# Optimization experiments

Hardware: AMD Instinct MI355X
Metric: run time of the kernel (lower is better)

Reference implementation:

```python
import jax, jax.numpy as jnp
import numpy as np

N, E, EE = 2048, 32768, 262144
CS, CZ, CG, NRBF = 384, 128, 16, 64
D_MIN, D_MAX = 0.0, 20.0
LN_EPS = 1e-5
EPS = 1e-8


def _p(key, shape, scale):
    return (jax.random.normal(key, shape, dtype=jnp.float32) * scale)


def setup_inputs() -> dict:
    key = jax.random.key(0)
    ks = jax.random.split(key, 40)
    inp = {
        "node_features": jax.random.normal(ks[0], (N, CS), dtype=jnp.float32),
        "node_trans": jax.random.normal(ks[1], (N, 3), dtype=jnp.float32) * 5.0,
        "dst_edge_features": jax.random.normal(ks[2], (E, CZ), dtype=jnp.float32),
        "dst_edge_index": jax.random.randint(ks[3], (2, E), 0, N),
        "src_edge_features": jax.random.normal(ks[4], (E, CZ), dtype=jnp.float32),
        "src_edge_index": jax.random.randint(ks[5], (2, E), 0, N),
        "edge_edge_index": jax.random.randint(ks[6], (2, EE), 0, E),
        # params (torch Linear math: y = x @ W + b, W stored [in,out])
        "w_nl": _p(ks[7], (CS, CG), 0.05), "b_nl": jnp.zeros((CG,), jnp.float32),
        "w_nr": _p(ks[8], (CS, CG), 0.05), "b_nr": jnp.zeros((CG,), jnp.float32),
        "g_dst": jnp.ones((CZ,), jnp.float32), "bt_dst": jnp.zeros((CZ,), jnp.float32),
        "g_src": jnp.ones((CZ,), jnp.float32), "bt_src": jnp.zeros((CZ,), jnp.float32),
        "w_ep": _p(ks[9], (CZ, CZ), 0.08), "b_ep": jnp.zeros((CZ,), jnp.float32),
        "w_eg": _p(ks[10], (CZ, CZ), 0.08), "b_eg": jnp.zeros((CZ,), jnp.float32),
        "w_dg": _p(ks[11], (CG * CG, CZ), 0.06), "b_dg": jnp.zeros((CZ,), jnp.float32),
        "w_dp": _p(ks[12], (NRBF, CZ), 0.1), "b_dp": jnp.zeros((CZ,), jnp.float32),
        "g_out": jnp.ones((CZ,), jnp.float32), "bt_out": jnp.zeros((CZ,), jnp.float32),
        "w_lo": _p(ks[13], (CZ, CZ), 0.08), "b_lo": jnp.zeros((CZ,), jnp.float32),
        "w_og": _p(ks[14], (CZ, CZ), 0.08), "b_og": jnp.zeros((CZ,), jnp.float32),
    }
    return inp


def _ln(x, g, b):
    m = jnp.mean(x, axis=-1, keepdims=True)
    v = jnp.mean(jnp.square(x - m), axis=-1, keepdims=True)
    return (x - m) * jax.lax.rsqrt(v + LN_EPS) * g + b


def _rbf(d):
    mu = jnp.linspace(D_MIN, D_MAX, NRBF)  # [NRBF]
    sigma = (D_MAX - D_MIN) / NRBF
    return jnp.exp(-jnp.square((d[:, None] - mu) / sigma))  # [EE, NRBF]


def reference(node_features, node_trans, dst_edge_features, dst_edge_index,
              src_edge_features, src_edge_index, edge_edge_index,
              w_nl, b_nl, w_nr, b_nr, g_dst, bt_dst, g_src, bt_src,
              w_ep, b_ep, w_eg, b_eg, w_dg, b_dg, w_dp, b_dp,
              g_out, bt_out, w_lo, b_lo, w_og, b_og):
    ee0 = edge_edge_index[0]  # index into dst edges
    ee1 = edge_edge_index[1]  # index into src edges
    n1 = src_edge_index[0][ee1]  # left node per edge-edge pair
    n2 = dst_edge_index[0][ee0]  # right node per edge-edge pair

    dst_ef = _ln(dst_edge_features, g_dst, bt_dst)
    src_ef = _ln(src_edge_features, g_src, bt_src)

    node_left = node_features @ w_nl + b_nl   # [N, CG]
    node_right = node_features @ w_nr + b_nr  # [N, CG]

    # per-pair outer product gate: [EE, CG*CG]
    edge3 = jnp.einsum('ei,ej->eij', node_left[n1], node_right[n2]).reshape(-1, CG * CG)
    edge3_gate = edge3 @ w_dg + b_dg  # [EE, CZ]

    diff = node_trans[n1] - node_trans[n2] + EPS
    dist = jnp.linalg.norm(diff, axis=-1)  # [EE]
    dist_feat = _rbf(dist) @ w_dp + b_dp   # [EE, CZ]
    edge3_features = jax.nn.sigmoid(edge3_gate) * dist_feat

    edge2 = jax.nn.sigmoid(src_ef @ w_eg + b_eg) * (src_ef @ w_ep + b_ep)  # [E, CZ]
    edge_update = edge2[ee0] * edge3_features  # [EE, CZ]
    edge_update = jax.ops.segment_sum(edge_update, ee0, num_segments=E)  # [E, CZ]

    edge_update = _ln(edge_update, g_out, bt_out)
    edge_update = edge_update @ w_lo + b_lo
    edge_update = edge_update * jax.nn.sigmoid(dst_ef @ w_og + b_og)
    return edge_update
```

## Files before the change

kernel.cpp:

```cpp
#include <hip/hip_runtime.h>
#include <hip/hip_bf16.h>
#include <math.h>

#define NN    2048
#define NE    32768
#define NP    262144
#define CS_   384
#define CZ_   128
#define CG_   16
#define NRBF_ 64

typedef __attribute__((ext_vector_type(8))) short bf16x8;
typedef __attribute__((ext_vector_type(4))) float f32x4;

__device__ __forceinline__ unsigned short f2bf(float f) {
  __hip_bfloat16 h = __float2bfloat16(f);
  union { __hip_bfloat16 h; unsigned short u; } cv; cv.h = h; return cv.u;
}
__device__ __forceinline__ float bfbits(unsigned short h) {
  return __uint_as_float((unsigned)h << 16);
}
__device__ __forceinline__ float sigf(float x) {
  return __builtin_amdgcn_rcpf(1.f + __expf(-x));
}

__global__ void k_nodeproj(const float* __restrict__ nf,
                           const float* __restrict__ wnl, const float* __restrict__ bnl,
                           const float* __restrict__ wnr, const float* __restrict__ bnr,
                           unsigned short* __restrict__ nl, unsigned short* __restrict__ nr) {
  const int n = blockIdx.x;
  const int t = threadIdx.x;
  if (t >= 32) return;
  const float* __restrict__ w = (t < 16) ? wnl : wnr;
  const int col = t & 15;
  const float* __restrict__ row = nf + (size_t)n * CS_;
  float acc = 0.f;
  #pragma unroll 8
  for (int k = 0; k < CS_; ++k) acc = fmaf(row[k], w[k * CG_ + col], acc);
  acc += (t < 16) ? bnl[col] : bnr[col];
  ((t < 16) ? nl : nr)[n * CG_ + col] = f2bf(acc);
}

__global__ void k_prep(const float* __restrict__ wdg, const float* __restrict__ wdp,
                       const float* __restrict__ weg, const float* __restrict__ wep,
                       const float* __restrict__ wlo, const float* __restrict__ wog,
                       unsigned short* __restrict__ frag) {
  const int idx = blockIdx.x * 256 + threadIdx.x;
  if (idx >= 180224) return;
  if (idx < 32768) {
    const int e = idx & 7, l = (idx >> 3) & 63, ks = (idx >> 9) & 7, n = idx >> 12;
    frag[idx] = f2bf(wdg[(size_t)(ks * 32 + (l >> 4) * 8 + e) * CZ_ + n * 16 + (l & 15)]);
  } else if (idx < 40960) {
    const int j = idx - 32768;
    const int e = j & 7, l = (j >> 3) & 63, ks2 = (j >> 9) & 1, n = j >> 10;
    frag[idx] = f2bf(wdp[(size_t)(ks2 * 32 + (l >> 4) * 8 + e) * CZ_ + n * 16 + (l & 15)]);
  } else if (idx < 172032) {
    const bool lo = idx >= 106496;
    const int j2 = (idx - 40960) & 65535;
    const int m = j2 >> 14;
    const float* __restrict__ mp = (m == 0) ? weg : (m == 1) ? wep : (m == 2) ? wlo : wog;
    const int j = j2 & 16383;
    const int e = j & 7, l = (j >> 3) & 63, ks = (j >> 9) & 3, n = j >> 11;
    const float v = mp[(size_t)(ks * 32 + (l >> 4) * 8 + e) * CZ_ + n * 16 + (l & 15)];
    const unsigned short h = f2bf(v);
    frag[idx] = lo ? f2bf(v - bfbits(h)) : h;
  } else {
    const int j = idx - 172032;
    const int e = j & 7, l = (j >> 3) & 63, ks2 = (j >> 9) & 1, n = j >> 10;
    const float v = wdp[(size_t)(ks2 * 32 + (l >> 4) * 8 + e) * CZ_ + n * 16 + (l & 15)];
    const unsigned short h = f2bf(v);
    frag[idx] = f2bf(v - bfbits(h));
  }
}

__global__ void k_hist(const int* __restrict__ ee, int* __restrict__ hist) {
  const int p = blockIdx.x * 256 + threadIdx.x;
  atomicAdd(&hist[ee[p]], 1);
}

__global__ __launch_bounds__(1024) void k_scan(int* __restrict__ hist,
                                               int* __restrict__ start) {
  __shared__ int tot[1024];
  const int t = threadIdx.x;
  const int base = t * 32;
  int s = 0;
  for (int k = 0; k < 32; ++k) s += hist[base + k];
  tot[t] = s;
  __syncthreads();
  for (int off = 1; off < 1024; off <<= 1) {
    int v = tot[t];
    int u = (t >= off) ? tot[t - off] : 0;
    __syncthreads();
    tot[t] = v + u;
    __syncthreads();
  }
  int run = (t == 0) ? 0 : tot[t - 1];
  for (int k = 0; k < 32; ++k) {
    const int h = hist[base + k];
    start[base + k] = run;
    run += h;
    hist[base + k] = 0;
  }
  if (t == 1023) start[32768] = run;
}

__global__ void k_scatter(const int* __restrict__ ee, const int* __restrict__ start,
                          int* __restrict__ cursor, int* __restrict__ perm) {
  const int p = blockIdx.x * 256 + threadIdx.x;
  const int e = ee[p];
  const int idx = atomicAdd(&cursor[e], 1);
  perm[start[e] + idx] = p;
}

__device__ __forceinline__ void ln_to_frag2(
    const float* __restrict__ src, const float* __restrict__ gam,
    const float* __restrict__ bet, int row0, int tid,
    unsigned short (* __restrict__ afh)[64][8],
    unsigned short (* __restrict__ afl)[64][8]) {
  const int r = tid >> 2, qt = tid & 3;
  const float* __restrict__ xp = src + (size_t)(row0 + r) * CZ_ + qt * 32;
  float v[32];
  #pragma unroll
  for (int j = 0; j < 8; ++j) {
    const float4 t4 = ((const float4*)xp)[j];
    v[4*j+0] = t4.x; v[4*j+1] = t4.y; v[4*j+2] = t4.z; v[4*j+3] = t4.w;
  }
  float sum = 0.f, sq = 0.f;
  #pragma unroll
  for (int q = 0; q < 32; ++q) { sum += v[q]; sq = fmaf(v[q], v[q], sq); }
  sum += __shfl_xor(sum, 1); sq += __shfl_xor(sq, 1);
  sum += __shfl_xor(sum, 2); sq += __shfl_xor(sq, 2);
  const float mean = sum * (1.f / CZ_);
  const float rstd = rsqrtf(sq * (1.f / CZ_) - mean * mean + 1e-5f);
  const int fb = (r >> 4) * 4 + qt;
  const int r15 = r & 15;
  #pragma unroll
  for (int g = 0; g < 4; ++g) {
    unsigned pkh[4], pkl[4];
    #pragma unroll
    for (int h2 = 0; h2 < 4; ++h2) {
      const int c0 = qt * 32 + g * 8 + 2 * h2;
      const float f0 = (v[g*8+2*h2]   - mean) * rstd * gam[c0]   + bet[c0];
      const float f1 = (v[g*8+2*h2+1] - mean) * rstd * gam[c0+1] + bet[c0+1];
      const unsigned short h0 = f2bf(f0), h1 = f2bf(f1);
      const unsigned short l0 = f2bf(f0 - bfbits(h0)), l1 = f2bf(f1 - bfbits(h1));
      pkh[h2] = (unsigned)h0 | ((unsigned)h1 << 16);
      pkl[h2] = (unsigned)l0 | ((unsigned)l1 << 16);
    }
    *(uint4*)&afh[fb][g * 16 + r15][0] = make_uint4(pkh[0], pkh[1], pkh[2], pkh[3]);
    *(uint4*)&afl[fb][g * 16 + r15][0] = make_uint4(pkl[0], pkl[1], pkl[2], pkl[3]);
  }
}

__global__ __launch_bounds__(256) void k_edge2_mfma(
    const float* __restrict__ sef,
    const float* __restrict__ gs, const float* __restrict__ bs,
    const unsigned short* __restrict__ wf,
    const float* __restrict__ beg, const float* __restrict__ bep,
    float* __restrict__ e2) {
  __shared__ unsigned short afh[16][64][8];
  __shared__ unsigned short afl[16][64][8];
  const int tid = threadIdx.x;
  const int row0 = blockIdx.x * 64;
  ln_to_frag2(sef, gs, bs, row0, tid, afh, afl);
  __syncthreads();

  const int lane = tid & 63;
  const int w = tid >> 6;
  f32x4 c1[8], c2[8];
  #pragma unroll
  for (int n = 0; n < 8; ++n) { c1[n] = (f32x4)0.f; c2[n] = (f32x4)0.f; }
  #pragma unroll
  for (int ks = 0; ks < 4; ++ks) {
    const bf16x8 ah = *(const bf16x8*)&afh[w * 4 + ks][lane][0];
    const bf16x8 al = *(const bf16x8*)&afl[w * 4 + ks][lane][0];
    #pragma unroll
    for (int n = 0; n < 8; ++n) {
      const size_t bo = ((size_t)((n * 4 + ks) * 64 + lane)) * 8;
      const bf16x8 b1h = *(const bf16x8*)(wf + bo);
      const bf16x8 b1l = *(const bf16x8*)(wf + 65536 + bo);
      const bf16x8 b2h = *(const bf16x8*)(wf + 16384 + bo);
      const bf16x8 b2l = *(const bf16x8*)(wf + 81920 + bo);
      c1[n] = __builtin_amdgcn_mfma_f32_16x16x32_bf16(ah, b1h, c1[n], 0, 0, 0);
      c1[n] = __builtin_amdgcn_mfma_f32_16x16x32_bf16(al, b1h, c1[n], 0, 0, 0);
      c1[n] = __builtin_amdgcn_mfma_f32_16x16x32_bf16(ah, b1l, c1[n], 0, 0, 0);
      c2[n] = __builtin_amdgcn_mfma_f32_16x16x32_bf16(ah, b2h, c2[n], 0, 0, 0);
      c2[n] = __builtin_amdgcn_mfma_f32_16x16x32_bf16(al, b2h, c2[n], 0, 0, 0);
      c2[n] = __builtin_amdgcn_mfma_f32_16x16x32_bf16(ah, b2l, c2[n], 0, 0, 0);
    }
  }
  const int c15 = lane & 15, rq = lane >> 4;
  #pragma unroll
  for (int n = 0; n < 8; ++n) {
    const int ch = n * 16 + c15;
    const float bg = beg[ch], bp = bep[ch];
    #pragma unroll
    for (int r = 0; r < 4; ++r) {
      const int row = row0 + w * 16 + rq * 4 + r;
      e2[(size_t)row * CZ_ + ch] = sigf(c1[n][r] + bg) * (c2[n][r] + bp);
    }
  }
}

template <int CC>
__global__ __launch_bounds__(256, 2) void k_pairfeat(
    const int* __restrict__ ee,
    const int* __restrict__ sei, const int* __restrict__ dei,
    const unsigned short* __restrict__ nlb, const unsigned short* __restrict__ nrb,
    const float* __restrict__ trans, const unsigned short* __restrict__ frag,
    const float* __restrict__ bdg, const float* __restrict__ bdp,
    float* __restrict__ feat) {
  __shared__ unsigned short sfrag[20480];
  const int tid = threadIdx.x;

  {
    const unsigned short* __restrict__ gsrc = frag + CC * 16384;
    #pragma unroll
    for (int i = 0; i < 8; ++i)
      ((float4*)sfrag)[i * 256 + tid] = ((const float4*)gsrc)[i * 256 + tid];
    const unsigned short* __restrict__ rsrc = frag + 32768 + CC * 4096;
    #pragma unroll
    for (int i = 0; i < 2; ++i)
      ((float4*)(sfrag + 16384))[i * 256 + tid] = ((const float4*)rsrc)[i * 256 + tid];
  }
  const unsigned short* __restrict__ wf2l = frag + 172032 + CC * 4096;

  const int lane = tid & 63;
  const int w = tid >> 6;
  const int g = lane >> 4;
  const int c15 = lane & 15;
  const int rowbase = blockIdx.x * 128 + w * 32;

  unsigned int nlu[2][8], nru[2][8];
  float dist[2];
  #pragma unroll
  for (int m = 0; m < 2; ++m) {
    const int p = rowbase + m * 16 + c15;
    const int e0 = ee[p];
    const int e1 = ee[NP + p];
    const int n1 = sei[e1];
    const int n2 = dei[e0];
    const uint4 a = ((const uint4*)(nlb + (size_t)n1 * CG_))[0];
    const uint4 b = ((const uint4*)(nlb + (size_t)n1 * CG_))[1];
    nlu[m][0]=a.x; nlu[m][1]=a.y; nlu[m][2]=a.z; nlu[m][3]=a.w;
    nlu[m][4]=b.x; nlu[m][5]=b.y; nlu[m][6]=b.z; nlu[m][7]=b.w;
    const uint4 c = ((const uint4*)(nrb + (size_t)n2 * CG_))[0];
    const uint4 d = ((const uint4*)(nrb + (size_t)n2 * CG_))[1];
    nru[m][0]=c.x; nru[m][1]=c.y; nru[m][2]=c.z; nru[m][3]=c.w;
    nru[m][4]=d.x; nru[m][5]=d.y; nru[m][6]=d.z; nru[m][7]=d.w;
    const float dx = trans[n1*3+0] - trans[n2*3+0] + 1e-8f;
    const float dy = trans[n1*3+1] - trans[n2*3+1] + 1e-8f;
    const float dz = trans[n1*3+2] - trans[n2*3+2] + 1e-8f;
    dist[m] = sqrtf(fmaf(dx, dx, fmaf(dy, dy, dz * dz)));
  }
  __syncthreads();

  f32x4 acc[2][4], acc2[2][4];
  #pragma unroll
  for (int m = 0; m < 2; ++m)
    #pragma unroll
    for (int n = 0; n < 4; ++n) { acc[m][n] = (f32x4)0.f; acc2[m][n] = (f32x4)0.f; }

  const bool hiI = (lane & 32) != 0;
  const bool hiJ = (lane & 16) != 0;

  #pragma unroll
  for (int ks = 0; ks < 8; ++ks) {
    bf16x8 af[2];
    #pragma unroll
    for (int m = 0; m < 2; ++m) {
      const unsigned wv = nlu[m][ks];
      const float nli = __uint_as_float(hiI ? (wv & 0xFFFF0000u) : (wv << 16));
      #pragma unroll
      for (int ep = 0; ep < 4; ++ep) {
        const unsigned wr = hiJ ? nru[m][4 + ep] : nru[m][ep];
        const float j0 = __uint_as_float(wr << 16);
        const float j1 = __uint_as_float(wr & 0xFFFF0000u);
        af[m][2*ep]   = (short)f2bf(nli * j0);
        af[m][2*ep+1] = (short)f2bf(nli * j1);
      }
    }
    #pragma unroll
    for (int n = 0; n < 4; ++n) {
      const bf16x8 bf = *(const bf16x8*)(sfrag + ((size_t)((n * 8 + ks) * 64 + lane)) * 8);
      acc[0][n] = __builtin_amdgcn_mfma_f32_16x16x32_bf16(af[0], bf, acc[0][n], 0, 0, 0);
      acc[1][n] = __builtin_amdgcn_mfma_f32_16x16x32_bf16(af[1], bf, acc[1][n], 0, 0, 0);
    }
  }

  const float MU_STEP = 20.f / 63.f;
  const float INV_SIG = 64.f / 20.f;
  #pragma unroll
  for (int ks2 = 0; ks2 < 2; ++ks2) {
    bf16x8 a2h[2], a2l[2];
    const int k2b = ks2 * 32 + g * 8;
    #pragma unroll
    for (int m = 0; m < 2; ++m) {
      #pragma unroll
      for (int e = 0; e < 8; ++e) {
        const float mu = (float)(k2b + e) * MU_STEP;
        const float u = (dist[m] - mu) * INV_SIG;
        const float ev = __expf(-u * u);
        const unsigned short h = f2bf(ev);
        a2h[m][e] = (short)h;
        a2l[m][e] = (short)f2bf(ev - bfbits(h));
      }
    }
    #pragma unroll
    for (int n = 0; n < 4; ++n) {
      const size_t bo = ((size_t)((n * 2 + ks2) * 64 + lane)) * 8;
      const bf16x8 b2h = *(const bf16x8*)(sfrag + 16384 + bo);
      const bf16x8 b2l = *(const bf16x8*)(wf2l + bo);
      acc2[0][n] = __builtin_amdgcn_mfma_f32_16x16x32_bf16(a2h[0], b2h, acc2[0][n], 0, 0, 0);
      acc2[0][n] = __builtin_amdgcn_mfma_f32_16x16x32_bf16(a2l[0], b2h, acc2[0][n], 0, 0, 0);
      acc2[0][n] = __builtin_amdgcn_mfma_f32_16x16x32_bf16(a2h[0], b2l, acc2[0][n], 0, 0, 0);
      acc2[1][n] = __builtin_amdgcn_mfma_f32_16x16x32_bf16(a2h[1], b2h, acc2[1][n], 0, 0, 0);
      acc2[1][n] = __builtin_amdgcn_mfma_f32_16x16x32_bf16(a2l[1], b2h, acc2[1][n], 0, 0, 0);
      acc2[1][n] = __builtin_amdgcn_mfma_f32_16x16x32_bf16(a2h[1], b2l, acc2[1][n], 0, 0, 0);
    }
  }

  float bdgv[4], bdpv[4];
  #pragma unroll
  for (int n = 0; n < 4; ++n) {
    bdgv[n] = bdg[(CC * 4 + n) * 16 + c15];
    bdpv[n] = bdp[(CC * 4 + n) * 16 + c15];
  }

  #pragma unroll
  for (int m = 0; m < 2; ++m) {
    #pragma unroll
    for (int n = 0; n < 4; ++n) {
      #pragma unroll
      for (int r = 0; r < 4; ++r) {
        const float gv = sigf(acc[m][n][r] + bdgv[n]);
        const int row = rowbase + m * 16 + g * 4 + r;
        feat[(size_t)row * 64 + n * 16 + c15] = gv * (acc2[m][n][r] + bdpv[n]);
      }
    }
  }
}

__global__ __launch_bounds__(64) void k_segsum(
    const int* __restrict__ start, const int* __restrict__ perm,
    const float* __restrict__ feat, float* __restrict__ e2, int cc) {
  __shared__ int lst[512];
  const int e = blockIdx.x;
  const int t = threadIdx.x;
  const int s0 = start[e], s1 = start[e + 1];
  const int deg = s1 - s0;
  float s = 0.f;
  if (deg <= 512) {
    for (int i = t; i < deg; i += 64) lst[i] = perm[s0 + i];
    __syncthreads();
    if (t == 0) {
      for (int a = 1; a < deg; ++a) {
        const int v = lst[a];
        int b = a - 1;
        while (b >= 0 && lst[b] > v) { lst[b + 1] = lst[b]; --b; }
        lst[b + 1] = v;
      }
    }
    __syncthreads();
    for (int j = 0; j < deg; ++j)
      s += feat[(size_t)lst[j] * 64 + t];
  } else {
    int last = -1;
    for (int j = 0; j < deg; ++j) {
      int mn = 0x7fffffff;
      for (int i = 0; i < deg; ++i) {
        const int p = perm[s0 + i];
        if (p > last && p < mn) mn = p;
      }
      last = mn;
      s += feat[(size_t)mn * 64 + t];
    }
  }
  float* __restrict__ dst = e2 + (size_t)e * CZ_ + cc * 64 + t;
  *dst = s * (*dst);
}

__global__ __launch_bounds__(256) void k_final_mfma(
    float* po, const float* __restrict__ def,
    const float* __restrict__ go, const float* __restrict__ bo,
    const float* __restrict__ gd, const float* __restrict__ bd,
    const unsigned short* __restrict__ wf,
    const float* __restrict__ blo, const float* __restrict__ bog) {
  __shared__ unsigned short af1h[16][64][8];
  __shared__ unsigned short af1l[16][64][8];
  __shared__ unsigned short af2h[16][64][8];
  __shared__ unsigned short af2l[16][64][8];
  const int tid = threadIdx.x;
  const int row0 = blockIdx.x * 64;
  ln_to_frag2(po, go, bo, row0, tid, af1h, af1l);
  ln_to_frag2(def, gd, bd, row0, tid, af2h, af2l);
  __syncthreads();

  const int lane = tid & 63;
  const int w = tid >> 6;
  f32x4 c1[8], c2[8];
  #pragma unroll
  for (int n = 0; n < 8; ++n) { c1[n] = (f32x4)0.f; c2[n] = (f32x4)0.f; }
  #pragma unroll
  for (int ks = 0; ks < 4; ++ks) {
    const bf16x8 a1h = *(const bf16x8*)&af1h[w * 4 + ks][lane][0];
    const bf16x8 a1l = *(const bf16x8*)&af1l[w * 4 + ks][lane][0];
    const bf16x8 a2h = *(const bf16x8*)&af2h[w * 4 + ks][lane][0];
    const bf16x8 a2l = *(const bf16x8*)&af2l[w * 4 + ks][lane][0];
    #pragma unroll
    for (int n = 0; n < 8; ++n) {
      const size_t bo = ((size_t)((n * 4 + ks) * 64 + lane)) * 8;
      const bf16x8 b1h = *(const bf16x8*)(wf + bo);
      const bf16x8 b1l = *(const bf16x8*)(wf + 65536 + bo);
      const bf16x8 b2h = *(const bf16x8*)(wf + 16384 + bo);
      const bf16x8 b2l = *(const bf16x8*)(wf + 81920 + bo);
      c1[n] = __builtin_amdgcn_mfma_f32_16x16x32_bf16(a1h, b1h, c1[n], 0, 0, 0);
      c1[n] = __builtin_amdgcn_mfma_f32_16x16x32_bf16(a1l, b1h, c1[n], 0, 0, 0);
      c1[n] = __builtin_amdgcn_mfma_f32_16x16x32_bf16(a1h, b1l, c1[n], 0, 0, 0);
      c2[n] = __builtin_amdgcn_mfma_f32_16x16x32_bf16(a2h, b2h, c2[n], 0, 0, 0);
      c2[n] = __builtin_amdgcn_mfma_f32_16x16x32_bf16(a2l, b2h, c2[n], 0, 0, 0);
      c2[n] = __builtin_amdgcn_mfma_f32_16x16x32_bf16(a2h, b2l, c2[n], 0, 0, 0);
    }
  }
  const int c15 = lane & 15, rq = lane >> 4;
  #pragma unroll
  for (int n = 0; n < 8; ++n) {
    const int ch = n * 16 + c15;
    const float bl = blo[ch], bg = bog[ch];
    #pragma unroll
    for (int r = 0; r < 4; ++r) {
      const int row = row0 + w * 16 + rq * 4 + r;
      po[(size_t)row * CZ_ + ch] = (c1[n][r] + bl) * sigf(c2[n][r] + bg);
    }
  }
}

extern "C" void kernel_launch(void* const* d_in, const int* in_sizes, int n_in,
                              void* d_out, int out_size, void* d_ws, size_t ws_size,
                              hipStream_t stream) {
  const float* nf     = (const float*)d_in[0];
  const float* trans  = (const float*)d_in[1];
  const float* dst_ef = (const float*)d_in[2];
  const int*   dst_ei = (const int*)d_in[3];
  const float* src_ef = (const float*)d_in[4];
  const int*   src_ei = (const int*)d_in[5];
  const int*   ee     = (const int*)d_in[6];
  const float* w_nl  = (const float*)d_in[7];  const float* b_nl  = (const float*)d_in[8];
  const float* w_nr  = (const float*)d_in[9];  const float* b_nr  = (const float*)d_in[10];
  const float* g_dst = (const float*)d_in[11]; const float* bt_dst= (const float*)d_in[12];
  const float* g_src = (const float*)d_in[13]; const float* bt_src= (const float*)d_in[14];
  const float* w_ep  = (const float*)d_in[15]; const float* b_ep  = (const float*)d_in[16];
  const float* w_eg  = (const float*)d_in[17]; const float* b_eg  = (const float*)d_in[18];
  const float* w_dg  = (const float*)d_in[19]; const float* b_dg  = (const float*)d_in[20];
  const float* w_dp  = (const float*)d_in[21]; const float* b_dp  = (const float*)d_in[22];
  const float* g_out = (const float*)d_in[23]; const float* bt_out= (const float*)d_in[24];
  const float* w_lo  = (const float*)d_in[25]; const float* b_lo  = (const float*)d_in[26];
  const float* w_og  = (const float*)d_in[27]; const float* b_og  = (const float*)d_in[28];

  float* e2 = (float*)d_out;

  char* ws = (char*)d_ws;
  size_t off = 0;
  float*        feat = (float*)(ws + off);        off += (size_t)NP * 64 * 4;
  unsigned short* nlb = (unsigned short*)(ws + off); off += (size_t)NN * CG_ * 2;
  unsigned short* nrb = (unsigned short*)(ws + off); off += (size_t)NN * CG_ * 2;
  unsigned short* frag = (unsigned short*)(ws + off); off += 180224 * 2;
  int* hist  = (int*)(ws + off); off += 32768 * 4;
  int* start = (int*)(ws + off); off += 32772 * 4;
  int* perm  = (int*)(ws + off); off += (size_t)NP * 4;

  const unsigned short* wf_pair = frag;
  const unsigned short* wf_e2   = frag + 40960;
  const unsigned short* wf_fin  = frag + 40960 + 32768;

  hipMemsetAsync(hist, 0, 32768 * 4, stream);

  k_nodeproj<<<NN, 64, 0, stream>>>(nf, w_nl, b_nl, w_nr, b_nr, nlb, nrb);
  k_prep<<<704, 256, 0, stream>>>(w_dg, w_dp, w_eg, w_ep, w_lo, w_og,
                                  (unsigned short*)frag);
  k_hist<<<NP / 256, 256, 0, stream>>>(ee, hist);
  k_scan<<<1, 1024, 0, stream>>>(hist, start);
  k_scatter<<<NP / 256, 256, 0, stream>>>(ee, start, hist, perm);
  k_edge2_mfma<<<NE / 64, 256, 0, stream>>>(src_ef, g_src, bt_src, wf_e2, b_eg, b_ep, e2);
  k_pairfeat<0><<<NP / 128, 256, 0, stream>>>(ee, src_ei, dst_ei, nlb, nrb, trans,
                                              wf_pair, b_dg, b_dp, feat);
  k_segsum<<<NE, 64, 0, stream>>>(start, perm, feat, e2, 0);
  k_pairfeat<1><<<NP / 128, 256, 0, stream>>>(ee, src_ei, dst_ei, nlb, nrb, trans,
                                              wf_pair, b_dg, b_dp, feat);
  k_segsum<<<NE, 64, 0, stream>>>(start, perm, feat, e2, 1);
  k_final_mfma<<<NE / 64, 256, 0, stream>>>(e2, dst_ef, g_out, bt_out, g_dst, bt_dst,
                                            wf_fin, b_lo, b_og);
}
```

Baseline: 244.0 us.

## Fuse segment sum into pair-feature kernel via sorted pairs and block partials

The pair-feature kernel now processes pairs in the order given by the sort permutation, so rows for the same edge are contiguous. It reduces them in shared memory with fixed-point int64 accumulation and writes fully contained segments straight into e2. Segments that cross block boundaries go to per-block partials, which a small fixup kernel combines. This removes the large feat buffer write and read, plus the per-edge insertion sort in the old segsum. In exchange it adds a serial 128-row scan by one wave per block and gathers the pair inputs through the permutation.

```diff
diff --git a/kernel.cpp b/kernel.cpp
--- a/kernel.cpp
+++ b/kernel.cpp
@@ -204,13 +204,15 @@
 
 template <int CC>
 __global__ __launch_bounds__(256, 2) void k_pairfeat(
-    const int* __restrict__ ee,
+    const int* __restrict__ perm, const int* __restrict__ ee,
     const int* __restrict__ sei, const int* __restrict__ dei,
     const unsigned short* __restrict__ nlb, const unsigned short* __restrict__ nrb,
     const float* __restrict__ trans, const unsigned short* __restrict__ frag,
     const float* __restrict__ bdg, const float* __restrict__ bdp,
-    float* __restrict__ feat) {
+    float* __restrict__ e2, long long* __restrict__ bpart, int* __restrict__ btag) {
   __shared__ unsigned short sfrag[20480];
+  __shared__ float tile[128][66];
+  __shared__ int es[128];
   const int tid = threadIdx.x;
 
   {
@@ -235,11 +237,13 @@
   float dist[2];
   #pragma unroll
   for (int m = 0; m < 2; ++m) {
-    const int p = rowbase + m * 16 + c15;
+    const int slot = rowbase + m * 16 + c15;
+    const int p = perm[slot];
     const int e0 = ee[p];
     const int e1 = ee[NP + p];
     const int n1 = sei[e1];
     const int n2 = dei[e0];
+    if (g == 0) es[w * 32 + m * 16 + c15] = e0;
     const uint4 a = ((const uint4*)(nlb + (size_t)n1 * CG_))[0];
     const uint4 b = ((const uint4*)(nlb + (size_t)n1 * CG_))[1];
     nlu[m][0]=a.x; nlu[m][1]=a.y; nlu[m][2]=a.z; nlu[m][3]=a.w;
@@ -334,50 +338,56 @@
       #pragma unroll
       for (int r = 0; r < 4; ++r) {
         const float gv = sigf(acc[m][n][r] + bdgv[n]);
-        const int row = rowbase + m * 16 + g * 4 + r;
-        feat[(size_t)row * 64 + n * 16 + c15] = gv * (acc2[m][n][r] + bdpv[n]);
+        tile[w * 32 + m * 16 + g * 4 + r][n * 16 + c15] = gv * (acc2[m][n][r] + bdpv[n]);
       }
     }
   }
-}
-
-__global__ __launch_bounds__(64) void k_segsum(
-    const int* __restrict__ start, const int* __restrict__ perm,
-    const float* __restrict__ feat, float* __restrict__ e2, int cc) {
-  __shared__ int lst[512];
+  __syncthreads();
+
+  if (tid < 64) {
+    const int ch = tid;
+    long long a = 0;
+    int cur = es[0], k = 0;
+    for (int r2 = 0; r2 < 128; ++r2) {
+      const int e = es[r2];
+      if (e != cur) {
+        if (k == 0) {
+          bpart[((size_t)blockIdx.x * 2) * 64 + ch] = a;
+          if (ch == 0) btag[blockIdx.x * 2] = cur;
+        } else {
+          float* dst = e2 + (size_t)cur * CZ_ + CC * 64 + ch;
+          *dst = (float)a * 0x1p-40f * (*dst);
+        }
+        ++k; a = 0; cur = e;
+      }
+      a += __float2ll_rn(tile[r2][ch] * 0x1p40f);
+    }
+    if (k == 0) {
+      bpart[((size_t)blockIdx.x * 2) * 64 + ch] = a;
+      if (ch == 0) { btag[blockIdx.x * 2] = cur; btag[blockIdx.x * 2 + 1] = -1; }
+    } else {
+      bpart[((size_t)blockIdx.x * 2 + 1) * 64 + ch] = a;
+      if (ch == 0) btag[blockIdx.x * 2 + 1] = cur;
+    }
+  }
+}
+
+__global__ __launch_bounds__(64) void k_fixup(
+    const int* __restrict__ start, const int* __restrict__ btag,
+    const long long* __restrict__ bpart, float* __restrict__ e2, int cc) {
   const int e = blockIdx.x;
   const int t = threadIdx.x;
   const int s0 = start[e], s1 = start[e + 1];
-  const int deg = s1 - s0;
-  float s = 0.f;
-  if (deg <= 512) {
-    for (int i = t; i < deg; i += 64) lst[i] = perm[s0 + i];
-    __syncthreads();
-    if (t == 0) {
-      for (int a = 1; a < deg; ++a) {
-        const int v = lst[a];
-        int b = a - 1;
-        while (b >= 0 && lst[b] > v) { lst[b + 1] = lst[b]; --b; }
-        lst[b + 1] = v;
-      }
-    }
-    __syncthreads();
-    for (int j = 0; j < deg; ++j)
-      s += feat[(size_t)lst[j] * 64 + t];
-  } else {
-    int last = -1;
-    for (int j = 0; j < deg; ++j) {
-      int mn = 0x7fffffff;
-      for (int i = 0; i < deg; ++i) {
-        const int p = perm[s0 + i];
-        if (p > last && p < mn) mn = p;
-      }
-      last = mn;
-      s += feat[(size_t)mn * 64 + t];
-    }
-  }
   float* __restrict__ dst = e2 + (size_t)e * CZ_ + cc * 64 + t;
-  *dst = s * (*dst);
+  if (s0 == s1) { *dst = 0.f; return; }
+  const int b0 = s0 >> 7, b1 = (s1 - 1) >> 7;
+  if (b0 == b1 && btag[2 * b0] != e && btag[2 * b0 + 1] != e) return;
+  long long sum = 0;
+  for (int b = b0; b <= b1; ++b) {
+    if (btag[2 * b]     == e) sum += bpart[((size_t)2 * b)     * 64 + t];
+    if (btag[2 * b + 1] == e) sum += bpart[((size_t)2 * b + 1) * 64 + t];
+  }
+  *dst = (float)sum * 0x1p-40f * (*dst);
 }
 
 __global__ __launch_bounds__(256) void k_final_mfma(
@@ -461,13 +471,14 @@
 
   char* ws = (char*)d_ws;
   size_t off = 0;
-  float*        feat = (float*)(ws + off);        off += (size_t)NP * 64 * 4;
   unsigned short* nlb = (unsigned short*)(ws + off); off += (size_t)NN * CG_ * 2;
   unsigned short* nrb = (unsigned short*)(ws + off); off += (size_t)NN * CG_ * 2;
   unsigned short* frag = (unsigned short*)(ws + off); off += 180224 * 2;
   int* hist  = (int*)(ws + off); off += 32768 * 4;
   int* start = (int*)(ws + off); off += 32772 * 4;
   int* perm  = (int*)(ws + off); off += (size_t)NP * 4;
+  int* btag  = (int*)(ws + off); off += 4096 * 4;
+  long long* bpart = (long long*)(ws + off); off += (size_t)4096 * 64 * 8;
 
   const unsigned short* wf_pair = frag;
   const unsigned short* wf_e2   = frag + 40960;
@@ -482,12 +493,12 @@
   k_scan<<<1, 1024, 0, stream>>>(hist, start);
   k_scatter<<<NP / 256, 256, 0, stream>>>(ee, start, hist, perm);
   k_edge2_mfma<<<NE / 64, 256, 0, stream>>>(src_ef, g_src, bt_src, wf_e2, b_eg, b_ep, e2);
-  k_pairfeat<0><<<NP / 128, 256, 0, stream>>>(ee, src_ei, dst_ei, nlb, nrb, trans,
-                                              wf_pair, b_dg, b_dp, feat);
-  k_segsum<<<NE, 64, 0, stream>>>(start, perm, feat, e2, 0);
-  k_pairfeat<1><<<NP / 128, 256, 0, stream>>>(ee, src_ei, dst_ei, nlb, nrb, trans,
-                                              wf_pair, b_dg, b_dp, feat);
-  k_segsum<<<NE, 64, 0, stream>>>(start, perm, feat, e2, 1);
+  k_pairfeat<0><<<NP / 128, 256, 0, stream>>>(perm, ee, src_ei, dst_ei, nlb, nrb, trans,
+                                              wf_pair, b_dg, b_dp, e2, bpart, btag);
+  k_fixup<<<NE, 64, 0, stream>>>(start, btag, bpart, e2, 0);
+  k_pairfeat<1><<<NP / 128, 256, 0, stream>>>(perm, ee, src_ei, dst_ei, nlb, nrb, trans,
+                                              wf_pair, b_dg, b_dp, e2, bpart, btag);
+  k_fixup<<<NE, 64, 0, stream>>>(start, btag, bpart, e2, 1);
   k_final_mfma<<<NE / 64, 256, 0, stream>>>(e2, dst_ef, g_out, bt_out, g_dst, bt_dst,
                                             wf_fin, b_lo, b_og);
 }
```

Measured after the change: 358.4 us. 46.9% more time.
